# Kernel optimization log

Measured on AMD Instinct MI355X. Metric: run time of the kernel, lower is better.

## Reference

```python
import jax, jax.numpy as jnp
import numpy as np

HIDDEN = 768
HEADS = 12
HEAD_DIM = HIDDEN // HEADS

def setup_inputs() -> dict:
    key = jax.random.key(0)
    ks = jax.random.split(key, 9)
    s = 1.0 / np.sqrt(HIDDEN)
    x = jax.random.normal(ks[0], (2, 2048, HIDDEN), dtype=jnp.float32)
    Wq = jax.random.normal(ks[1], (HIDDEN, HIDDEN), dtype=jnp.float32) * s
    bq = jnp.zeros((HIDDEN,), dtype=jnp.float32)
    Wk = jax.random.normal(ks[2], (HIDDEN, HIDDEN), dtype=jnp.float32) * s
    bk = jnp.zeros((HIDDEN,), dtype=jnp.float32)
    Wv = jax.random.normal(ks[3], (HIDDEN, HIDDEN), dtype=jnp.float32) * s
    bv = jnp.zeros((HIDDEN,), dtype=jnp.float32)
    Wo = jax.random.normal(ks[4], (HIDDEN, HIDDEN), dtype=jnp.float32) * s
    bo = jnp.zeros((HIDDEN,), dtype=jnp.float32)
    return {"x": x, "Wq": Wq, "bq": bq, "Wk": Wk, "bk": bk,
            "Wv": Wv, "bv": bv, "Wo": Wo, "bo": bo}

def reference(x, Wq, bq, Wk, bk, Wv, bv, Wo, bo):
    B, S, _ = x.shape
    # project and split heads: [B, H, S, D]
    def proj(W, b):
        return (x @ W + b).reshape(B, S, HEADS, HEAD_DIM).transpose(0, 2, 1, 3)
    q = proj(Wq, bq)
    k = proj(Wk, bk)
    v = proj(Wv, bv)
    # NOTE: original module does NOT scale by 1/sqrt(head_dim)
    scores = jnp.einsum('bhqd,bhkd->bhqk', q, k)
    attn = jax.nn.softmax(scores, axis=-1)
    out = jnp.einsum('bhqk,bhkd->bhqd', attn, v)
    out = out.transpose(0, 2, 1, 3).reshape(B, S, HIDDEN)
    return out @ Wo + bo
```

## Files before the change

kernel.cpp:

```cpp
#include <hip/hip_runtime.h>
#include <cstddef>

#define HIDDEN 768
#define NHEADS 12
#define HDIM   64
#define BATCH  2
#define SEQ    2048
#define NROWS  (BATCH*SEQ)
#define LOG2E  1.4426950408889634f

typedef float f32x4  __attribute__((ext_vector_type(4)));
typedef float f32x16 __attribute__((ext_vector_type(16)));
typedef short bf16x8 __attribute__((ext_vector_type(8)));

__device__ __forceinline__ float fast_exp2(float x){
    return __builtin_amdgcn_exp2f(x);
}

__device__ __forceinline__ unsigned short f2bf(float f){
    unsigned u = __builtin_bit_cast(unsigned, f);
    u = u + 0x7FFFu + ((u >> 16) & 1u);
    return (unsigned short)(u >> 16);
}
__device__ __forceinline__ unsigned packbf2(float a, float b){
    unsigned ua = (__builtin_bit_cast(unsigned, a) + 0x8000u) >> 16;
    unsigned ub = (__builtin_bit_cast(unsigned, b) + 0x8000u) & 0xFFFF0000u;
    return ua | ub;
}
__device__ __forceinline__ unsigned cvtpk_bf16(float a, float b){
    unsigned r;
    asm("v_cvt_pk_bf16_f32 %0, %1, %2" : "=v"(r) : "v"(a), "v"(b));
    return r;
}

__device__ __forceinline__ void gl_lds16(const unsigned short* g, unsigned short* l){
    __builtin_amdgcn_global_load_lds(
        (const __attribute__((address_space(1))) unsigned int*)g,
        (__attribute__((address_space(3))) unsigned int*)l, 16, 0, 0);
}

__global__ __launch_bounds__(256) void cvt_bf16(const float* __restrict__ in,
                                                unsigned short* __restrict__ out,
                                                int n4)
{
    const int i = blockIdx.x * 256 + threadIdx.x;
    if (i >= n4) return;
    const float4 v = reinterpret_cast<const float4*>(in)[i];
    ushort4 o;
    o.x = f2bf(v.x); o.y = f2bf(v.y); o.z = f2bf(v.z); o.w = f2bf(v.w);
    reinterpret_cast<ushort4*>(out)[i] = o;
}

__global__ __launch_bounds__(256) void transpose_cvt4(const float* __restrict__ W0,
                                                      const float* __restrict__ W1,
                                                      const float* __restrict__ W2,
                                                      const float* __restrict__ W3,
                                                      unsigned short* __restrict__ T0,
                                                      unsigned short* __restrict__ T1,
                                                      unsigned short* __restrict__ T2,
                                                      unsigned short* __restrict__ T3)
{
    const int z = blockIdx.z;
    const float* W = (z == 0) ? W0 : (z == 1) ? W1 : (z == 2) ? W2 : W3;
    unsigned short* Wt = (z == 0) ? T0 : (z == 1) ? T1 : (z == 2) ? T2 : T3;

    __shared__ unsigned short t[64][66];
    const int k0 = blockIdx.y * 64, n0 = blockIdx.x * 64;
    const int row = threadIdx.x >> 2;
    const int c0  = (threadIdx.x & 3) * 16;
#pragma unroll
    for (int j = 0; j < 16; j += 4) {
        const float4 v = *reinterpret_cast<const float4*>(&W[(size_t)(k0 + row) * HIDDEN + n0 + c0 + j]);
        t[row][c0 + j + 0] = f2bf(v.x);
        t[row][c0 + j + 1] = f2bf(v.y);
        t[row][c0 + j + 2] = f2bf(v.z);
        t[row][c0 + j + 3] = f2bf(v.w);
    }
    __syncthreads();
#pragma unroll
    for (int j = 0; j < 16; j += 4) {
        ushort4 o;
        o.x = t[c0 + j + 0][row];
        o.y = t[c0 + j + 1][row];
        o.z = t[c0 + j + 2][row];
        o.w = t[c0 + j + 3][row];
        *reinterpret_cast<ushort4*>(&Wt[(size_t)(n0 + row) * HIDDEN + k0 + c0 + j]) = o;
    }
}

__device__ __forceinline__ void gemm_body(const unsigned short* __restrict__ A,
                                          const unsigned short* __restrict__ Wt,
                                          const float* __restrict__ bias,
                                          void* __restrict__ Cout, int mode,
                                          float scale,
                                          unsigned short* As, unsigned short* Bs)
{
    const int tid = threadIdx.x;
    const int l = tid & 63, w = tid >> 6;
    const int wm = w >> 1, wn = w & 1;
    const int l15 = l & 15, lg = l >> 4;
    const int srow = l >> 3, sslot = l & 7;
    const int m0 = blockIdx.y * 64, n0 = blockIdx.x * 96;

    f32x4 acc[2][3] = {};

    for (int k0 = 0; k0 < HIDDEN; k0 += 64) {
        __syncthreads();
#pragma unroll
        for (int a = 0; a < 2; ++a) {
            const int row = (a * 4 + w) * 8 + srow;
            const int sl = sslot ^ (row & 7);
            gl_lds16(&A[(size_t)(m0 + row) * HIDDEN + k0 + sl * 8], &As[(a * 4 + w) * 512]);
        }
#pragma unroll
        for (int b = 0; b < 3; ++b) {
            const int row = (b * 4 + w) * 8 + srow;
            const int sl = sslot ^ (row & 7);
            gl_lds16(&Wt[(size_t)(n0 + row) * HIDDEN + k0 + sl * 8], &Bs[(b * 4 + w) * 512]);
        }
        __syncthreads();

#pragma unroll
        for (int kk = 0; kk < 2; ++kk) {
            bf16x8 af[2], bfr[3];
#pragma unroll
            for (int mi = 0; mi < 2; ++mi) {
                const int r = wm * 32 + mi * 16 + l15;
                af[mi] = *reinterpret_cast<const bf16x8*>(&As[r * 64 + ((lg * 8 + kk * 32) ^ ((r & 7) << 3))]);
            }
#pragma unroll
            for (int ni = 0; ni < 3; ++ni) {
                const int r = wn * 48 + ni * 16 + l15;
                bfr[ni] = *reinterpret_cast<const bf16x8*>(&Bs[r * 64 + ((lg * 8 + kk * 32) ^ ((r & 7) << 3))]);
            }
#pragma unroll
            for (int mi = 0; mi < 2; ++mi)
#pragma unroll
                for (int ni = 0; ni < 3; ++ni)
                    acc[mi][ni] = __builtin_amdgcn_mfma_f32_16x16x32_bf16(af[mi], bfr[ni], acc[mi][ni], 0, 0, 0);
        }
    }

#pragma unroll
    for (int mi = 0; mi < 2; ++mi) {
#pragma unroll
        for (int ni = 0; ni < 3; ++ni) {
#pragma unroll
            for (int rr = 0; rr < 4; ++rr) {
                const int row = m0 + wm * 32 + mi * 16 + lg * 4 + rr;
                const int col = n0 + wn * 48 + ni * 16 + l15;
                const float v = (acc[mi][ni][rr] + bias[col]) * scale;
                if (mode == 0) {
                    const int b = row >> 11, s = row & (SEQ - 1);
                    const int hh = col >> 6, d = col & (HDIM - 1);
                    ((unsigned short*)Cout)[(((size_t)b * NHEADS + hh) * SEQ + s) * HDIM + d] = f2bf(v);
                } else if (mode == 1) {
                    const int b = row >> 11, s = row & (SEQ - 1);
                    const int hh = col >> 6, d = col & (HDIM - 1);
                    ((unsigned short*)Cout)[(((size_t)b * NHEADS + hh) * HDIM + d) * SEQ + s] = f2bf(v);
                } else {
                    ((float*)Cout)[(size_t)row * HIDDEN + col] = v;
                }
            }
        }
    }
}

__global__ __launch_bounds__(256) void qkv_gemm(const unsigned short* __restrict__ A,
                                                const unsigned short* __restrict__ Wqt,
                                                const unsigned short* __restrict__ Wkt,
                                                const unsigned short* __restrict__ Wvt,
                                                const float* __restrict__ bq,
                                                const float* __restrict__ bk,
                                                const float* __restrict__ bv,
                                                unsigned short* __restrict__ Qb,
                                                unsigned short* __restrict__ Kb,
                                                unsigned short* __restrict__ Vtb)
{
    __shared__ unsigned short As[64 * 64];
    __shared__ unsigned short Bs[96 * 64];
    const int z = blockIdx.z;
    const unsigned short* Wt = (z == 0) ? Wqt : (z == 1) ? Wkt : Wvt;
    const float* bias = (z == 0) ? bq : (z == 1) ? bk : bv;
    void* out = (z == 0) ? (void*)Qb : (z == 1) ? (void*)Kb : (void*)Vtb;
    const int mode = (z == 2) ? 1 : 0;
    const float scale = (z == 0) ? LOG2E : 1.0f;
    gemm_body(A, Wt, bias, out, mode, scale, As, Bs);
}

__global__ __launch_bounds__(256) void out_gemm(const unsigned short* __restrict__ A,
                                                const unsigned short* __restrict__ Wt,
                                                const float* __restrict__ bias,
                                                float* __restrict__ Cout)
{
    __shared__ unsigned short As[64 * 64];
    __shared__ unsigned short Bs[96 * 64];
    gemm_body(A, Wt, bias, Cout, 2, 1.0f, As, Bs);
}

__global__ __launch_bounds__(256) void attn_mfma(const unsigned short* __restrict__ Q,
                                                 const unsigned short* __restrict__ K,
                                                 const unsigned short* __restrict__ Vt,
                                                 unsigned short* __restrict__ O)
{
    __shared__ __align__(16) char shraw[33792];
    unsigned short* Ks  = (unsigned short*)shraw;
    unsigned short* Vs  = (unsigned short*)(shraw + 16384);
    float*          xch = (float*)shraw;
    unsigned int*   Ep  = (unsigned int*)(shraw + 16384);
    float2*         mlx = (float2*)(shraw + 32768);

    const int tid = threadIdx.x;
    const int l = tid & 63;
    const int wq2 = (tid >> 6) & 1;
    const int wkv = tid >> 7;
    const int l31 = l & 31, hi = l >> 5;
    const int lr = l >> 3, slot = l & 7;
    const int q0 = blockIdx.x * 64;
    const int h = blockIdx.y, b = blockIdx.z;
    const size_t base = ((size_t)b * NHEADS + h) * (size_t)SEQ * HDIM;

    const int q = q0 + wq2 * 32 + l31;
    bf16x8 qf[4];
#pragma unroll
    for (int t = 0; t < 4; ++t)
        qf[t] = *reinterpret_cast<const bf16x8*>(&Q[base + (size_t)q * HDIM + 16 * t + 8 * hi]);

    f32x16 accO[2] = {};
    float m = -1e30f, lsum = 0.f;

    unsigned short* Kb = Ks + wkv * 4096;
    unsigned short* Vb = Vs + wkv * 4096;
    const int kvbase = wkv * (SEQ / 2);

    for (int i = 0; i < SEQ / 128; ++i) {
        const int t0 = kvbase + i * 64;
        __syncthreads();
#pragma unroll
        for (int j = 0; j < 4; ++j) {
            const int row = (j * 2 + wq2) * 8 + lr;
            const int sl = slot ^ (row & 7);
            gl_lds16(&K [base + (size_t)(t0 + row) * HDIM + sl * 8], &Kb[(j * 2 + wq2) * 512]);
            gl_lds16(&Vt[base + (size_t)row * SEQ + t0 + sl * 8],    &Vb[(j * 2 + wq2) * 512]);
        }
        __syncthreads();

        f32x16 s0v = {}, s1v = {};
        __builtin_amdgcn_s_setprio(1);
#pragma unroll
        for (int t = 0; t < 4; ++t) {
            const int co = 16 * t + 8 * hi;
            const int r0 = l31, r1 = 32 + l31;
            const bf16x8 k0 = *reinterpret_cast<const bf16x8*>(&Kb[r0 * 64 + (co ^ ((r0 & 7) << 3))]);
            const bf16x8 k1 = *reinterpret_cast<const bf16x8*>(&Kb[r1 * 64 + (co ^ ((r1 & 7) << 3))]);
            s0v = __builtin_amdgcn_mfma_f32_32x32x16_bf16(k0, qf[t], s0v, 0, 0, 0);
            s1v = __builtin_amdgcn_mfma_f32_32x32x16_bf16(k1, qf[t], s1v, 0, 0, 0);
        }
        __builtin_amdgcn_s_setprio(0);

        float tmax = -1e30f;
#pragma unroll
        for (int r = 0; r < 16; r += 4) {
            tmax = fmaxf(tmax, fmaxf(fmaxf(s0v[r], s0v[r + 1]), fmaxf(s0v[r + 2], s0v[r + 3])));
            tmax = fmaxf(tmax, fmaxf(fmaxf(s1v[r], s1v[r + 1]), fmaxf(s1v[r + 2], s1v[r + 3])));
        }
        tmax = fmaxf(tmax, __shfl_xor(tmax, 32));

        if (tmax > m + 8.f) {
            const float scl = fast_exp2(m - tmax);
            lsum *= scl;
#pragma unroll
            for (int r = 0; r < 16; ++r) { accO[0][r] *= scl; accO[1][r] *= scl; }
            m = tmax;
        }

        unsigned wv[16];
        float ls = 0.f;
#pragma unroll
        for (int a = 0; a < 8; ++a) {
            const float pa = fast_exp2(s0v[2 * a] - m);
            const float pb = fast_exp2(s0v[2 * a + 1] - m);
            ls += pa + pb;
            wv[a] = cvtpk_bf16(pa, pb);
        }
#pragma unroll
        for (int a = 0; a < 8; ++a) {
            const float pa = fast_exp2(s1v[2 * a] - m);
            const float pb = fast_exp2(s1v[2 * a + 1] - m);
            ls += pa + pb;
            wv[8 + a] = cvtpk_bf16(pa, pb);
        }
        ls += __shfl_xor(ls, 32);
        lsum += ls;

#pragma unroll
        for (int slot2 = 0; slot2 < 4; ++slot2) {
            const unsigned w0 = wv[slot2 * 4 + 0], w1 = wv[slot2 * 4 + 1];
            const unsigned w2 = wv[slot2 * 4 + 2], w3 = wv[slot2 * 4 + 3];
            const unsigned x0 = (unsigned)__shfl_xor((int)w0, 32);
            const unsigned x1 = (unsigned)__shfl_xor((int)w1, 32);
            const unsigned x2 = (unsigned)__shfl_xor((int)w2, 32);
            const unsigned x3 = (unsigned)__shfl_xor((int)w3, 32);
            uint4 fr;
            fr.x = hi ? x2 : w0;
            fr.y = hi ? x3 : w1;
            fr.z = hi ? w2 : x0;
            fr.w = hi ? w3 : x1;
            const bf16x8 pfrag = __builtin_bit_cast(bf16x8, fr);
            __builtin_amdgcn_s_setprio(1);
#pragma unroll
            for (int db = 0; db < 2; ++db) {
                const int vr = 32 * db + l31;
                const int co = (16 * slot2 + 8 * hi) ^ ((vr & 7) << 3);
                const bf16x8 vf = *reinterpret_cast<const bf16x8*>(&Vb[vr * 64 + co]);
                accO[db] = __builtin_amdgcn_mfma_f32_32x32x16_bf16(vf, pfrag, accO[db], 0, 0, 0);
            }
            __builtin_amdgcn_s_setprio(0);
        }
    }

    __syncthreads();
    if (!hi) mlx[(wq2 * 2 + wkv) * 32 + l31] = make_float2(m, lsum);
    __syncthreads();
    const float2 mp = mlx[(wq2 * 2 + (1 - wkv)) * 32 + l31];
    const float M  = fmaxf(m, mp.x);
    const float s  = fast_exp2(m - M);
    const float lf = lsum * s + mp.y * fast_exp2(mp.x - M);

    if (wkv == 1) {
#pragma unroll
        for (int db = 0; db < 2; ++db)
#pragma unroll
            for (int r = 0; r < 16; ++r) {
                const int d = 32 * db + (r & 3) + 8 * (r >> 2) + 4 * hi;
                xch[wq2 * 2048 + d * 32 + l31] = accO[db][r] * s;
            }
    }
    __syncthreads();
    if (wkv == 0) {
        const float inv = 1.f / lf;
#pragma unroll
        for (int db = 0; db < 2; ++db)
#pragma unroll
            for (int r = 0; r < 16; ++r) {
                const int d = 32 * db + (r & 3) + 8 * (r >> 2) + 4 * hi;
                accO[db][r] = (accO[db][r] * s + xch[wq2 * 2048 + d * 32 + l31]) * inv;
            }
#pragma unroll
        for (int db = 0; db < 2; ++db)
#pragma unroll
            for (int a = 0; a < 8; ++a) {
                const unsigned wd = packbf2(accO[db][2 * a], accO[db][2 * a + 1]);
                const int pi = 16 * db + 4 * (a >> 1) + (a & 1) + 2 * hi;
                Ep[(wq2 * 32 + l31) * 33 + pi] = wd;
            }
    }
    __syncthreads();
    if (wkv == 0) {
#pragma unroll
        for (int pss = 0; pss < 4; ++pss) {
            const int idx = pss * 64 + l;
            const int qr = idx >> 3, c = idx & 7;
            uint4 ov;
            ov.x = Ep[(wq2 * 32 + qr) * 33 + c * 4 + 0];
            ov.y = Ep[(wq2 * 32 + qr) * 33 + c * 4 + 1];
            ov.z = Ep[(wq2 * 32 + qr) * 33 + c * 4 + 2];
            ov.w = Ep[(wq2 * 32 + qr) * 33 + c * 4 + 3];
            *reinterpret_cast<uint4*>(&O[((size_t)b * SEQ + q0 + wq2 * 32 + qr) * HIDDEN + h * HDIM + c * 8]) = ov;
        }
    }
}

extern "C" void kernel_launch(void* const* d_in, const int* in_sizes, int n_in,
                              void* d_out, int out_size, void* d_ws, size_t ws_size,
                              hipStream_t stream)
{
    const float* x  = (const float*)d_in[0];
    const float* Wq = (const float*)d_in[1];
    const float* bq = (const float*)d_in[2];
    const float* Wk = (const float*)d_in[3];
    const float* bk = (const float*)d_in[4];
    const float* Wv = (const float*)d_in[5];
    const float* bv = (const float*)d_in[6];
    const float* Wo = (const float*)d_in[7];
    const float* bo = (const float*)d_in[8];
    float* out = (float*)d_out;

    unsigned short* p = (unsigned short*)d_ws;
    const size_t szX = (size_t)NROWS * HIDDEN;
    const size_t szW = (size_t)HIDDEN * HIDDEN;
    const size_t szH = (size_t)BATCH * NHEADS * SEQ * HDIM;
    unsigned short* xb  = p;              p += szX;
    unsigned short* Wqt = p;              p += szW;
    unsigned short* Wkt = p;              p += szW;
    unsigned short* Wvt = p;              p += szW;
    unsigned short* Wot = p;              p += szW;
    unsigned short* Qb  = p;              p += szH;
    unsigned short* Kb  = p;              p += szH;
    unsigned short* Vtb = p;              p += szH;
    unsigned short* Oab = p;              p += szX;

    cvt_bf16<<<(int)(szX / 4 + 255) / 256, 256, 0, stream>>>(x, xb, (int)(szX / 4));
    transpose_cvt4<<<dim3(HIDDEN / 64, HIDDEN / 64, 4), 256, 0, stream>>>(
        Wq, Wk, Wv, Wo, Wqt, Wkt, Wvt, Wot);

    qkv_gemm<<<dim3(HIDDEN / 96, NROWS / 64, 3), 256, 0, stream>>>(
        xb, Wqt, Wkt, Wvt, bq, bk, bv, Qb, Kb, Vtb);

    attn_mfma<<<dim3(SEQ / 64, NHEADS, BATCH), 256, 0, stream>>>(Qb, Kb, Vtb, Oab);

    out_gemm<<<dim3(HIDDEN / 96, NROWS / 64), 256, 0, stream>>>(Oab, Wot, bo, out);
}
```

Measured before the change: 112.1 us.

## Split attention KV across four independent waves per 32-query block

Restructures the attention kernel so each block handles 32 queries and each of its four waves processes a private quarter of the key/value sequence, with no block-wide barriers inside the loop. Each wave loads its own K and V tiles into private LDS and waits only on its own memory counters. The four partial softmax states are merged at the end through LDS. The grid doubles, and launch bounds now request four blocks per CU. This removes per-iteration __syncthreads stalls and raises occupancy, but K/V reuse per block is halved and each load is exposed with no overlap.

```diff
diff --git a/kernel.cpp b/kernel.cpp
--- a/kernel.cpp
+++ b/kernel.cpp
@@ -198,29 +198,28 @@
     gemm_body(A, Wt, bias, Cout, 2, 1.0f, As, Bs);
 }
 
-__global__ __launch_bounds__(256) void attn_mfma(const unsigned short* __restrict__ Q,
-                                                 const unsigned short* __restrict__ K,
-                                                 const unsigned short* __restrict__ Vt,
-                                                 unsigned short* __restrict__ O)
-{
-    __shared__ __align__(16) char shraw[33792];
-    unsigned short* Ks  = (unsigned short*)shraw;
-    unsigned short* Vs  = (unsigned short*)(shraw + 16384);
-    float*          xch = (float*)shraw;
-    unsigned int*   Ep  = (unsigned int*)(shraw + 16384);
-    float2*         mlx = (float2*)(shraw + 32768);
+__global__ __launch_bounds__(256, 4) void attn_mfma(const unsigned short* __restrict__ Q,
+                                                    const unsigned short* __restrict__ K,
+                                                    const unsigned short* __restrict__ Vt,
+                                                    unsigned short* __restrict__ O)
+{
+    __shared__ __align__(16) char shraw[32768];
+    unsigned short* shus = (unsigned short*)shraw;
+    float*          pub  = (float*)shraw;
+    float2*         mlx  = (float2*)(shraw + 24576);
+    unsigned int*   Ep   = (unsigned int*)shraw;
 
     const int tid = threadIdx.x;
-    const int l = tid & 63;
-    const int wq2 = (tid >> 6) & 1;
-    const int wkv = tid >> 7;
+    const int l = tid & 63, w = tid >> 6;
     const int l31 = l & 31, hi = l >> 5;
-    const int lr = l >> 3, slot = l & 7;
-    const int q0 = blockIdx.x * 64;
+    const int q0 = blockIdx.x * 32;
     const int h = blockIdx.y, b = blockIdx.z;
     const size_t base = ((size_t)b * NHEADS + h) * (size_t)SEQ * HDIM;
 
-    const int q = q0 + wq2 * 32 + l31;
+    unsigned short* Kb = shus + w * 4096;
+    unsigned short* Vb = Kb + 2048;
+
+    const int q = q0 + l31;
     bf16x8 qf[4];
 #pragma unroll
     for (int t = 0; t < 4; ++t)
@@ -229,41 +228,40 @@
     f32x16 accO[2] = {};
     float m = -1e30f, lsum = 0.f;
 
-    unsigned short* Kb = Ks + wkv * 4096;
-    unsigned short* Vb = Vs + wkv * 4096;
-    const int kvbase = wkv * (SEQ / 2);
-
-    for (int i = 0; i < SEQ / 128; ++i) {
-        const int t0 = kvbase + i * 64;
-        __syncthreads();
-#pragma unroll
-        for (int j = 0; j < 4; ++j) {
-            const int row = (j * 2 + wq2) * 8 + lr;
-            const int sl = slot ^ (row & 7);
-            gl_lds16(&K [base + (size_t)(t0 + row) * HDIM + sl * 8], &Kb[(j * 2 + wq2) * 512]);
-            gl_lds16(&Vt[base + (size_t)row * SEQ + t0 + sl * 8],    &Vb[(j * 2 + wq2) * 512]);
-        }
-        __syncthreads();
-
-        f32x16 s0v = {}, s1v = {};
+    const int klr = l >> 3, kslot = l & 7;
+    const int vdl = l & 15, vjs = l >> 4;
+
+    for (int t = 0; t < 16; ++t) {
+        const int t0 = w * (SEQ / 4) + t * 32;
+
+        asm volatile("s_waitcnt lgkmcnt(0)" ::: "memory");
+#pragma unroll
+        for (int c = 0; c < 4; ++c) {
+            const int row = c * 8 + klr;
+            const int sl = kslot ^ (row & 7);
+            gl_lds16(&K[base + (size_t)(t0 + row) * HDIM + sl * 8], &Kb[c * 512]);
+        }
+#pragma unroll
+        for (int c = 0; c < 4; ++c) {
+            gl_lds16(&Vt[base + (size_t)(c * 16 + vdl) * SEQ + t0 + vjs * 8], &Vb[c * 512]);
+        }
+        asm volatile("s_waitcnt vmcnt(0)" ::: "memory");
+        __builtin_amdgcn_sched_barrier(0);
+
+        f32x16 sv = {};
         __builtin_amdgcn_s_setprio(1);
 #pragma unroll
-        for (int t = 0; t < 4; ++t) {
-            const int co = 16 * t + 8 * hi;
-            const int r0 = l31, r1 = 32 + l31;
-            const bf16x8 k0 = *reinterpret_cast<const bf16x8*>(&Kb[r0 * 64 + (co ^ ((r0 & 7) << 3))]);
-            const bf16x8 k1 = *reinterpret_cast<const bf16x8*>(&Kb[r1 * 64 + (co ^ ((r1 & 7) << 3))]);
-            s0v = __builtin_amdgcn_mfma_f32_32x32x16_bf16(k0, qf[t], s0v, 0, 0, 0);
-            s1v = __builtin_amdgcn_mfma_f32_32x32x16_bf16(k1, qf[t], s1v, 0, 0, 0);
+        for (int tt = 0; tt < 4; ++tt) {
+            const int co = 16 * tt + 8 * hi;
+            const bf16x8 kf = *reinterpret_cast<const bf16x8*>(&Kb[l31 * 64 + (co ^ ((l31 & 7) << 3))]);
+            sv = __builtin_amdgcn_mfma_f32_32x32x16_bf16(kf, qf[tt], sv, 0, 0, 0);
         }
         __builtin_amdgcn_s_setprio(0);
 
         float tmax = -1e30f;
 #pragma unroll
-        for (int r = 0; r < 16; r += 4) {
-            tmax = fmaxf(tmax, fmaxf(fmaxf(s0v[r], s0v[r + 1]), fmaxf(s0v[r + 2], s0v[r + 3])));
-            tmax = fmaxf(tmax, fmaxf(fmaxf(s1v[r], s1v[r + 1]), fmaxf(s1v[r + 2], s1v[r + 3])));
-        }
+        for (int r = 0; r < 16; r += 4)
+            tmax = fmaxf(tmax, fmaxf(fmaxf(sv[r], sv[r + 1]), fmaxf(sv[r + 2], sv[r + 3])));
         tmax = fmaxf(tmax, __shfl_xor(tmax, 32));
 
         if (tmax > m + 8.f) {
@@ -274,29 +272,22 @@
             m = tmax;
         }
 
-        unsigned wv[16];
+        unsigned wv[8];
         float ls = 0.f;
 #pragma unroll
         for (int a = 0; a < 8; ++a) {
-            const float pa = fast_exp2(s0v[2 * a] - m);
-            const float pb = fast_exp2(s0v[2 * a + 1] - m);
+            const float pa = fast_exp2(sv[2 * a] - m);
+            const float pb = fast_exp2(sv[2 * a + 1] - m);
             ls += pa + pb;
             wv[a] = cvtpk_bf16(pa, pb);
         }
-#pragma unroll
-        for (int a = 0; a < 8; ++a) {
-            const float pa = fast_exp2(s1v[2 * a] - m);
-            const float pb = fast_exp2(s1v[2 * a + 1] - m);
-            ls += pa + pb;
-            wv[8 + a] = cvtpk_bf16(pa, pb);
-        }
         ls += __shfl_xor(ls, 32);
         lsum += ls;
 
 #pragma unroll
-        for (int slot2 = 0; slot2 < 4; ++slot2) {
-            const unsigned w0 = wv[slot2 * 4 + 0], w1 = wv[slot2 * 4 + 1];
-            const unsigned w2 = wv[slot2 * 4 + 2], w3 = wv[slot2 * 4 + 3];
+        for (int s2 = 0; s2 < 2; ++s2) {
+            const unsigned w0 = wv[s2 * 4 + 0], w1 = wv[s2 * 4 + 1];
+            const unsigned w2 = wv[s2 * 4 + 2], w3 = wv[s2 * 4 + 3];
             const unsigned x0 = (unsigned)__shfl_xor((int)w0, 32);
             const unsigned x1 = (unsigned)__shfl_xor((int)w1, 32);
             const unsigned x2 = (unsigned)__shfl_xor((int)w2, 32);
@@ -310,9 +301,10 @@
             __builtin_amdgcn_s_setprio(1);
 #pragma unroll
             for (int db = 0; db < 2; ++db) {
-                const int vr = 32 * db + l31;
-                const int co = (16 * slot2 + 8 * hi) ^ ((vr & 7) << 3);
-                const bf16x8 vf = *reinterpret_cast<const bf16x8*>(&Vb[vr * 64 + co]);
+                const int d = 32 * db + l31;
+                const int js = 2 * s2 + hi;
+                const bf16x8 vf = *reinterpret_cast<const bf16x8*>(
+                    &Vb[(d >> 4) * 512 + (js * 16 + (d & 15)) * 8]);
                 accO[db] = __builtin_amdgcn_mfma_f32_32x32x16_bf16(vf, pfrag, accO[db], 0, 0, 0);
             }
             __builtin_amdgcn_s_setprio(0);
@@ -320,53 +312,66 @@
     }
 
     __syncthreads();
-    if (!hi) mlx[(wq2 * 2 + wkv) * 32 + l31] = make_float2(m, lsum);
+    if (!hi) mlx[w * 32 + l31] = make_float2(m, lsum);
     __syncthreads();
-    const float2 mp = mlx[(wq2 * 2 + (1 - wkv)) * 32 + l31];
-    const float M  = fmaxf(m, mp.x);
-    const float s  = fast_exp2(m - M);
-    const float lf = lsum * s + mp.y * fast_exp2(mp.x - M);
-
-    if (wkv == 1) {
+    float M = -1e30f;
+    float mj[4], lj[4];
+#pragma unroll
+    for (int j = 0; j < 4; ++j) {
+        const float2 tml = mlx[j * 32 + l31];
+        mj[j] = tml.x; lj[j] = tml.y;
+        M = fmaxf(M, tml.x);
+    }
+    float lf = 0.f;
+#pragma unroll
+    for (int j = 0; j < 4; ++j) lf += lj[j] * fast_exp2(mj[j] - M);
+    const float s = fast_exp2(m - M);
+    const float inv = 1.f / lf;
+
+    if (w != 0) {
 #pragma unroll
         for (int db = 0; db < 2; ++db)
 #pragma unroll
             for (int r = 0; r < 16; ++r) {
                 const int d = 32 * db + (r & 3) + 8 * (r >> 2) + 4 * hi;
-                xch[wq2 * 2048 + d * 32 + l31] = accO[db][r] * s;
+                pub[(w - 1) * 2048 + l31 * 64 + ((d + l31) & 63)] = accO[db][r] * s;
             }
     }
     __syncthreads();
-    if (wkv == 0) {
-        const float inv = 1.f / lf;
+    if (w == 0) {
 #pragma unroll
         for (int db = 0; db < 2; ++db)
 #pragma unroll
             for (int r = 0; r < 16; ++r) {
                 const int d = 32 * db + (r & 3) + 8 * (r >> 2) + 4 * hi;
-                accO[db][r] = (accO[db][r] * s + xch[wq2 * 2048 + d * 32 + l31]) * inv;
-            }
+                float v = accO[db][r] * s;
+#pragma unroll
+                for (int wi = 0; wi < 3; ++wi)
+                    v += pub[wi * 2048 + l31 * 64 + ((d + l31) & 63)];
+                accO[db][r] = v * inv;
+            }
+        asm volatile("s_waitcnt lgkmcnt(0)" ::: "memory");
+        __builtin_amdgcn_sched_barrier(0);
 #pragma unroll
         for (int db = 0; db < 2; ++db)
 #pragma unroll
             for (int a = 0; a < 8; ++a) {
                 const unsigned wd = packbf2(accO[db][2 * a], accO[db][2 * a + 1]);
                 const int pi = 16 * db + 4 * (a >> 1) + (a & 1) + 2 * hi;
-                Ep[(wq2 * 32 + l31) * 33 + pi] = wd;
-            }
-    }
-    __syncthreads();
-    if (wkv == 0) {
+                Ep[l31 * 33 + pi] = wd;
+            }
+        asm volatile("s_waitcnt lgkmcnt(0)" ::: "memory");
+        __builtin_amdgcn_sched_barrier(0);
 #pragma unroll
         for (int pss = 0; pss < 4; ++pss) {
             const int idx = pss * 64 + l;
             const int qr = idx >> 3, c = idx & 7;
             uint4 ov;
-            ov.x = Ep[(wq2 * 32 + qr) * 33 + c * 4 + 0];
-            ov.y = Ep[(wq2 * 32 + qr) * 33 + c * 4 + 1];
-            ov.z = Ep[(wq2 * 32 + qr) * 33 + c * 4 + 2];
-            ov.w = Ep[(wq2 * 32 + qr) * 33 + c * 4 + 3];
-            *reinterpret_cast<uint4*>(&O[((size_t)b * SEQ + q0 + wq2 * 32 + qr) * HIDDEN + h * HDIM + c * 8]) = ov;
+            ov.x = Ep[qr * 33 + c * 4 + 0];
+            ov.y = Ep[qr * 33 + c * 4 + 1];
+            ov.z = Ep[qr * 33 + c * 4 + 2];
+            ov.w = Ep[qr * 33 + c * 4 + 3];
+            *reinterpret_cast<uint4*>(&O[((size_t)b * SEQ + q0 + qr) * HIDDEN + h * HDIM + c * 8]) = ov;
         }
     }
 }
@@ -407,7 +412,7 @@
     qkv_gemm<<<dim3(HIDDEN / 96, NROWS / 64, 3), 256, 0, stream>>>(
         xb, Wqt, Wkt, Wvt, bq, bk, bv, Qb, Kb, Vtb);
 
-    attn_mfma<<<dim3(SEQ / 64, NHEADS, BATCH), 256, 0, stream>>>(Qb, Kb, Vtb, Oab);
+    attn_mfma<<<dim3(SEQ / 32, NHEADS, BATCH), 256, 0, stream>>>(Qb, Kb, Vtb, Oab);
 
     out_gemm<<<dim3(HIDDEN / 96, NROWS / 64), 256, 0, stream>>>(Oab, Wot, bo, out);
 }
```

New measurement: 123.9 us. +10.5%, slower.

## Prefetch next K/V tile into registers to overlap global loads with compute

Applied to the files above, without the earlier changes.

Replaces the direct global-to-LDS loads with register staging. The next K and V tiles are loaded into registers while the current tile is being computed, then written to LDS at the start of the next iteration. The aim is to hide global memory latency behind the MFMA and softmax work. The cost is extra VGPR pressure, which may lower occupancy, plus an explicit LDS store pass.

```diff
diff --git a/kernel.cpp b/kernel.cpp
--- a/kernel.cpp
+++ b/kernel.cpp
@@ -233,16 +233,29 @@
     unsigned short* Vb = Vs + wkv * 4096;
     const int kvbase = wkv * (SEQ / 2);
 
+    uint4 kr[4], vr[4];
+#define LOADKV(T0) do {                                                                       \
+    _Pragma("unroll")                                                                         \
+    for (int j_ = 0; j_ < 4; ++j_) {                                                          \
+        const int row_ = (j_ * 2 + wq2) * 8 + lr;                                             \
+        const int sl_ = slot ^ (row_ & 7);                                                    \
+        kr[j_] = *reinterpret_cast<const uint4*>(&K [base + (size_t)((T0) + row_) * HDIM + sl_ * 8]); \
+        vr[j_] = *reinterpret_cast<const uint4*>(&Vt[base + (size_t)row_ * SEQ + (T0) + sl_ * 8]);   \
+    }                                                                                         \
+} while (0)
+#define WRITEKV() do {                                                                        \
+    _Pragma("unroll")                                                                         \
+    for (int j_ = 0; j_ < 4; ++j_) {                                                          \
+        *reinterpret_cast<uint4*>(&Kb[(j_ * 2 + wq2) * 512 + l * 8]) = kr[j_];                \
+        *reinterpret_cast<uint4*>(&Vb[(j_ * 2 + wq2) * 512 + l * 8]) = vr[j_];                \
+    }                                                                                         \
+} while (0)
+
+    LOADKV(kvbase);
     for (int i = 0; i < SEQ / 128; ++i) {
-        const int t0 = kvbase + i * 64;
         __syncthreads();
-#pragma unroll
-        for (int j = 0; j < 4; ++j) {
-            const int row = (j * 2 + wq2) * 8 + lr;
-            const int sl = slot ^ (row & 7);
-            gl_lds16(&K [base + (size_t)(t0 + row) * HDIM + sl * 8], &Kb[(j * 2 + wq2) * 512]);
-            gl_lds16(&Vt[base + (size_t)row * SEQ + t0 + sl * 8],    &Vb[(j * 2 + wq2) * 512]);
-        }
+        WRITEKV();
+        if (i + 1 < SEQ / 128) LOADKV(kvbase + (i + 1) * 64);
         __syncthreads();
 
         f32x16 s0v = {}, s1v = {};
@@ -310,14 +323,16 @@
             __builtin_amdgcn_s_setprio(1);
 #pragma unroll
             for (int db = 0; db < 2; ++db) {
-                const int vr = 32 * db + l31;
-                const int co = (16 * slot2 + 8 * hi) ^ ((vr & 7) << 3);
-                const bf16x8 vf = *reinterpret_cast<const bf16x8*>(&Vb[vr * 64 + co]);
+                const int vrr = 32 * db + l31;
+                const int co = (16 * slot2 + 8 * hi) ^ ((vrr & 7) << 3);
+                const bf16x8 vf = *reinterpret_cast<const bf16x8*>(&Vb[vrr * 64 + co]);
                 accO[db] = __builtin_amdgcn_mfma_f32_32x32x16_bf16(vf, pfrag, accO[db], 0, 0, 0);
             }
             __builtin_amdgcn_s_setprio(0);
         }
     }
+#undef LOADKV
+#undef WRITEKV
 
     __syncthreads();
     if (!hi) mlx[(wq2 * 2 + wkv) * 32 + l31] = make_float2(m, lsum);
```

Measured after the change: 184.3 us. 1.64x slower.
